# Performance work log

Measured on AMD Instinct MI355X. Metric: run time of the kernel, lower is better.

Reference implementation:

```python
import jax, jax.numpy as jnp
import numpy as np

EPS = 1e-5
PATCH_LEN, STRIDE, SEQ_LEN = 16, 8, 512
D_FF, N_HEADS = 32, 8


def setup_inputs() -> dict:
    key = jax.random.key(0)
    ks = jax.random.split(key, 16)
    d_model, d_llm, V, num_tok, pred_len = 32, 4096, 32000, 1000, 96
    hf = N_HEADS * D_FF  # 256
    patch_nums = (SEQ_LEN - PATCH_LEN) // STRIDE + 2  # 64
    head_nf = D_FF * patch_nums  # 2048
    r = lambda k, s, fan: jax.random.normal(k, s, jnp.float32) / np.sqrt(fan)
    return {
        'x_enc': jax.random.normal(ks[0], (32, SEQ_LEN, 7), jnp.float32),
        'conv_w': r(ks[1], (d_model, PATCH_LEN, 3), PATCH_LEN * 3),
        'word_emb': jax.random.normal(ks[2], (V, d_llm), jnp.float32) * 0.02,
        'map_w': r(ks[3], (num_tok, V), V),
        'map_b': jnp.zeros((num_tok,), jnp.float32),
        'wq': r(ks[4], (hf, d_model), d_model), 'bq': jnp.zeros((hf,), jnp.float32),
        'wk': r(ks[5], (hf, d_llm), d_llm), 'bk': jnp.zeros((hf,), jnp.float32),
        'wv': r(ks[6], (hf, d_llm), d_llm), 'bv': jnp.zeros((hf,), jnp.float32),
        'wo': r(ks[7], (d_llm, hf), hf), 'bo': jnp.zeros((d_llm,), jnp.float32),
        'head_w': r(ks[8], (pred_len, head_nf), head_nf),
        'head_b': jnp.zeros((pred_len,), jnp.float32),
    }


def _forward(x_enc, conv_w, word_emb, map_w, map_b, wq, bq, wk, bk, wv, bv, wo, bo, head_w, head_b):
    B, T, N = x_enc.shape
    # RevIN normalize (stats detached, as in torch)
    mean = jax.lax.stop_gradient(jnp.mean(x_enc, axis=1, keepdims=True))
    stdev = jax.lax.stop_gradient(jnp.sqrt(jnp.var(x_enc, axis=1, keepdims=True) + EPS))
    x = (x_enc - mean) / stdev                      # [B,T,N]

    # Patch embedding: [B,N,T] -> replication pad -> unfold -> circular conv
    xt = jnp.transpose(x, (0, 2, 1))                # [B,N,T]
    xt = jnp.concatenate([xt, jnp.repeat(xt[..., -1:], STRIDE, axis=-1)], axis=-1)  # [B,N,T+stride]
    starts = jnp.arange(0, T + STRIDE - PATCH_LEN + 1, STRIDE)
    idx = starts[:, None] + jnp.arange(PATCH_LEN)   # [L, patch_len]
    patches = xt[:, :, idx]                         # [B,N,L,patch_len]
    L = patches.shape[2]
    p = patches.reshape(B * N, L, PATCH_LEN)
    # TokenEmbedding: conv1d over patch axis, circular pad 1, no bias
    pc = jnp.transpose(p, (0, 2, 1))                # [BN, patch_len, L]
    pc = jnp.concatenate([pc[..., -1:], pc, pc[..., :1]], axis=-1)
    emb = jax.lax.conv_general_dilated(pc, conv_w, (1,), 'VALID',
                                       dimension_numbers=('NCH', 'OIH', 'NCH'))
    enc = jnp.transpose(emb, (0, 2, 1))             # [BN, L, d_model]

    # Source embeddings: mapping_layer(word_emb.T).T -> [num_tokens, d_llm]
    src = (word_emb.T @ map_w.T + map_b).T          # [num_tok, d_llm]

    # Reprogramming cross-attention
    BN = enc.shape[0]
    q = (enc @ wq.T + bq).reshape(BN, L, N_HEADS, D_FF)   # [BN,L,H,E]
    k = (src @ wk.T + bk).reshape(-1, N_HEADS, D_FF)      # [S,H,E]
    v = (src @ wv.T + bv).reshape(-1, N_HEADS, D_FF)      # [S,H,E]
    scale = 1.0 / np.sqrt(D_FF)
    scores = jnp.einsum('blhe,she->bhls', q, k)
    A = jax.nn.softmax(scale * scores, axis=-1)
    rep = jnp.einsum('bhls,she->blhe', A, v).reshape(BN, L, N_HEADS * D_FF)
    out = rep @ wo.T + bo                           # [BN, L, d_llm]

    # LLM stubbed as identity; keep first d_ff channels (Time-LLM post-LLM path)
    dec = out[..., :D_FF]                           # [BN, L, d_ff]
    dec = dec.reshape(B, N, L, D_FF).transpose(0, 1, 3, 2)  # [B,N,d_ff,L]
    dec = dec.reshape(B, N, D_FF * L)               # FlattenHead
    dec = dec @ head_w.T + head_b                   # [B,N,pred_len]
    dec = jnp.transpose(dec, (0, 2, 1))             # [B,pred_len,N]
    # RevIN denormalize
    return dec * stdev + mean


def reference(x_enc, conv_w, word_emb, map_w, map_b, wq, bq, wk, bk, wv, bv, wo, bo, head_w, head_b):
    return _forward(x_enc, conv_w, word_emb, map_w, map_b, wq, bq, wk, bk, wv, bv, wo, bo, head_w, head_b)
```

## Files before the change

### kernel.cpp

```cpp
#include <hip/hip_runtime.h>
#include <math.h>

constexpr int B_ = 32, T_ = 512, N_ = 7, BN_ = 224;
constexpr int L_ = 64, DM_ = 32, PLEN_ = 16;
constexpr int HF_ = 256, NH_ = 8, DFF_ = 32;
constexpr int S_ = 1000, SP_ = 1024, DLLM_ = 4096, V_ = 32000;
constexpr int PRED_ = 96, HNF_ = 2048;
constexpr int KSPLIT2 = 25, KCH2 = 1280;

typedef short bf16x8 __attribute__((ext_vector_type(8)));
typedef float f32x4 __attribute__((ext_vector_type(4)));

__device__ inline ushort f2bf(float x) {
    union { float f; uint u; } v; v.f = x;
    uint r = v.u + 0x7fffu + ((v.u >> 16) & 1u);
    return (ushort)(r >> 16);
}
__device__ inline uint pk(float a, float b) {
    return (uint)f2bf(a) | ((uint)f2bf(b) << 16);
}
__device__ inline void gl16(const void* g, void* l) {
    __builtin_amdgcn_global_load_lds(
        (const __attribute__((address_space(1))) void*)g,
        (__attribute__((address_space(3))) void*)l, 16, 0, 0);
}

__global__ __launch_bounds__(256) void k_pre(const float* __restrict__ x,
                                             const float* __restrict__ conv_w,
                                             const float* __restrict__ wq,
                                             const float* __restrict__ bq,
                                             float* __restrict__ mean_o,
                                             float* __restrict__ std_o,
                                             float* __restrict__ qo) {
    const int bn = blockIdx.x, b = bn / N_, n = bn % N_;
    __shared__ float xn[520];
    __shared__ float cw[DM_ * PLEN_ * 3];
    __shared__ float enc_s[2048];
    __shared__ float wqs[HF_ * DM_];
    __shared__ float rs[4], rq[4], sm2[2];
    const int tid = threadIdx.x;
    const float* xp = x + (size_t)b * T_ * N_ + n;

    float s = 0.f, sq = 0.f;
    for (int t = tid; t < T_; t += 256) { float v = xp[(size_t)t * N_]; s += v; sq += v * v; }
    for (int i = tid; i < DM_ * PLEN_ * 3; i += 256) cw[i] = conv_w[i];
    for (int i = tid; i < HF_ * DM_; i += 256) wqs[i] = wq[i];
    for (int o = 32; o > 0; o >>= 1) { s += __shfl_down(s, o, 64); sq += __shfl_down(sq, o, 64); }
    int wid = tid >> 6, lane = tid & 63;
    if (lane == 0) { rs[wid] = s; rq[wid] = sq; }
    __syncthreads();
    if (tid == 0) {
        float S = rs[0] + rs[1] + rs[2] + rs[3];
        float Q = rq[0] + rq[1] + rq[2] + rq[3];
        float m = S / T_;
        float var = Q / T_ - m * m;
        float sd = sqrtf(var + 1e-5f);
        mean_o[bn] = m; std_o[bn] = sd;
        sm2[0] = m; sm2[1] = sd;
    }
    __syncthreads();
    const float m = sm2[0], rstd = 1.0f / sm2[1];
    for (int t = tid; t < T_; t += 256) xn[t] = (xp[(size_t)t * N_] - m) * rstd;
    __syncthreads();
    if (tid < 8) xn[T_ + tid] = xn[T_ - 1];
    __syncthreads();
    for (int idx = tid; idx < L_ * DM_ * 8; idx += 256) { }
    for (int idx = tid; idx < L_ * DM_; idx += 256) {
        int l = idx >> 5, o = idx & 31;
        float acc = 0.f;
        #pragma unroll
        for (int t = 0; t < 3; t++) {
            int col = l + t;
            int pcol = (col == 0) ? 63 : ((col == 65) ? 0 : col - 1);
            const float* xb = &xn[pcol * 8];
            const float* cwb = &cw[o * 48 + t];
            #pragma unroll
            for (int i = 0; i < 16; i++) acc += xb[i] * cwb[i * 3];
        }
        enc_s[idx] = acc;
    }
    __syncthreads();
    const float scale = 0.17677669529663687f;
    for (int idx = tid; idx < L_ * HF_; idx += 256) {
        int l = idx >> 8, c = idx & 255;
        float acc = bq[c];
        const float* e = &enc_s[l * 32];
        const float* w = &wqs[c * 32];
        #pragma unroll
        for (int k = 0; k < 32; k++) acc += e[k] * w[k];
        qo[(size_t)bn * L_ * HF_ + idx] = acc * scale;
    }
}

__global__ __launch_bounds__(256) void k_wsum(const float* __restrict__ wk,
                                              const float* __restrict__ wv,
                                              float* __restrict__ wsum) {
    int c = blockIdx.x;
    const float* row = (c < HF_) ? wk + (size_t)c * DLLM_ : wv + (size_t)(c - HF_) * DLLM_;
    float s = 0.f;
    for (int d = threadIdx.x; d < DLLM_; d += 256) s += row[d];
    for (int o = 32; o > 0; o >>= 1) s += __shfl_down(s, o, 64);
    __shared__ float rs[4];
    int wid = threadIdx.x >> 6, lane = threadIdx.x & 63;
    if (lane == 0) rs[wid] = s;
    __syncthreads();
    if (threadIdx.x == 0) wsum[c] = rs[0] + rs[1] + rs[2] + rs[3];
}

__global__ __launch_bounds__(256) void k_cvt_wkv(const float* __restrict__ wk,
                                                 const float* __restrict__ wv,
                                                 ushort* __restrict__ out) {
    int g = blockIdx.x * 256 + threadIdx.x;
    int e = g * 8;
    const float* src = (e < HF_ * DLLM_) ? wk + e : wv + (e - HF_ * DLLM_);
    float4 x = *(const float4*)src, y = *(const float4*)(src + 4);
    uint4 w; w.x = pk(x.x, x.y); w.y = pk(x.z, x.w); w.z = pk(y.x, y.y); w.w = pk(y.z, y.w);
    *(uint4*)(out + e) = w;
}

__global__ __launch_bounds__(512) void k_gemm1(const float* __restrict__ A,
                                               const ushort* __restrict__ Bw,
                                               ushort* __restrict__ ET) {
    __shared__ union {
        struct { float Af[2][128 * 32]; ushort Bs[2][256 * 32]; } st;
        ushort C[256 * 72];
    } lds;
    const int tid = threadIdx.x;
    const int lane = tid & 63, wid = tid >> 6;
    const int wr = wid >> 2, wc = wid & 3;
    const int n0 = blockIdx.x * 256, m0 = blockIdx.y * 128;

    const int arw = tid >> 3, acq = (tid & 7) ^ ((tid >> 3) & 7);
    const float* asrc0 = A + (size_t)(m0 + arw) * DLLM_ + acq * 4;
    const float* asrc1 = asrc0 + (size_t)64 * DLLM_;

    const int u0 = tid, rb0 = u0 >> 2, ob0 = (u0 & 3) ^ ((rb0 >> 1) & 3);
    const int u1 = tid + 512, rb1 = u1 >> 2, ob1 = (u1 & 3) ^ ((rb1 >> 1) & 3);
    const ushort* bptr0 = Bw + (size_t)(n0 + rb0) * DLLM_ + ob0 * 8;
    const ushort* bptr1 = Bw + (size_t)(n0 + rb1) * DLLM_ + ob1 * 8;

    const int rl = lane & 15, g = lane >> 4;
    const int oc = g ^ ((rl >> 1) & 3);

    f32x4 acc[4][4];
    #pragma unroll
    for (int i = 0; i < 4; i++)
        #pragma unroll
        for (int j = 0; j < 4; j++) acc[i][j] = (f32x4){0.f, 0.f, 0.f, 0.f};

    gl16(asrc0, &lds.st.Af[0][tid * 4]);
    gl16(asrc1, &lds.st.Af[0][(tid + 512) * 4]);
    gl16(bptr0, &lds.st.Bs[0][u0 * 8]);
    gl16(bptr1, &lds.st.Bs[0][u1 * 8]);
    __syncthreads();

    int cur = 0;
    constexpr int NT = DLLM_ / 32;
    for (int t = 0; t < NT; ++t) {
        if (t + 1 < NT) {
            const int o = (t + 1) * 32;
            gl16(asrc0 + o, &lds.st.Af[cur ^ 1][tid * 4]);
            gl16(asrc1 + o, &lds.st.Af[cur ^ 1][(tid + 512) * 4]);
            gl16(bptr0 + o, &lds.st.Bs[cur ^ 1][u0 * 8]);
            gl16(bptr1 + o, &lds.st.Bs[cur ^ 1][u1 * 8]);
            asm volatile("s_waitcnt vmcnt(4)" ::: "memory");
        } else {
            asm volatile("s_waitcnt vmcnt(0)" ::: "memory");
        }
        __builtin_amdgcn_s_barrier();
        asm volatile("" ::: "memory");
        const float* Ab = lds.st.Af[cur];
        const ushort* Bb = lds.st.Bs[cur];
        bf16x8 af[4], bfr[4];
        #pragma unroll
        for (int mi = 0; mi < 4; mi++) {
            int row = wr * 64 + mi * 16 + rl;
            int s = row & 7;
            int ulo = row * 8 + ((2 * g) ^ s);
            int uhi = row * 8 + ((2 * g + 1) ^ s);
            f32x4 xlo = *(const f32x4*)&Ab[ulo * 4];
            f32x4 xhi = *(const f32x4*)&Ab[uhi * 4];
            uint4 w; w.x = pk(xlo[0], xlo[1]); w.y = pk(xlo[2], xlo[3]);
            w.z = pk(xhi[0], xhi[1]); w.w = pk(xhi[2], xhi[3]);
            union { uint4 u; bf16x8 b; } cv; cv.u = w;
            af[mi] = cv.b;
        }
        #pragma unroll
        for (int ni = 0; ni < 4; ni++)
            bfr[ni] = *(const bf16x8*)&Bb[(wc * 64 + ni * 16 + rl) * 32 + oc * 8];
        __builtin_amdgcn_s_setprio(1);
        #pragma unroll
        for (int mi = 0; mi < 4; mi++)
            #pragma unroll
            for (int ni = 0; ni < 4; ni++)
                acc[mi][ni] = __builtin_amdgcn_mfma_f32_16x16x32_bf16(af[mi], bfr[ni], acc[mi][ni], 0, 0, 0);
        __builtin_amdgcn_s_setprio(0);
        asm volatile("s_waitcnt lgkmcnt(0)" ::: "memory");
        __builtin_amdgcn_s_barrier();
        cur ^= 1;
    }

    #pragma unroll
    for (int p = 0; p < 2; p++) {
        __syncthreads();
        if (wr == p) {
            #pragma unroll
            for (int mi = 0; mi < 4; mi++)
                #pragma unroll
                for (int ni = 0; ni < 4; ni++) {
                    int nl = wc * 64 + ni * 16 + (lane & 15);
                    int ml = mi * 16 + (lane >> 4) * 4;
                    uint2 w2;
                    w2.x = pk(acc[mi][ni][0], acc[mi][ni][1]);
                    w2.y = pk(acc[mi][ni][2], acc[mi][ni][3]);
                    *(uint2*)&lds.C[nl * 72 + ml] = w2;
                }
        }
        __syncthreads();
        {
            int r = tid >> 1, half = tid & 1;
            const uint4* src = (const uint4*)&lds.C[r * 72 + half * 32];
            ushort* dst = ET + (size_t)(n0 + r) * V_ + m0 + p * 64 + half * 32;
            uint4 v0 = src[0], v1 = src[1], v2 = src[2], v3 = src[3];
            *(uint4*)(dst + 0) = v0; *(uint4*)(dst + 8) = v1;
            *(uint4*)(dst + 16) = v2; *(uint4*)(dst + 24) = v3;
        }
    }
}

__global__ __launch_bounds__(256) void k_gemm2(const float* __restrict__ A,
                                               const ushort* __restrict__ ET,
                                               float* __restrict__ Cp) {
    __shared__ float Af[2][128 * 32];
    __shared__ ushort Bs[2][128 * 32];
    const int tid = threadIdx.x, lane = tid & 63, wid = tid >> 6;
    const int wr = wid >> 1, wc = wid & 1;
    const int m0 = blockIdx.x * 128, n0 = blockIdx.y * 128, kz = blockIdx.z;
    const size_t kbase = (size_t)kz * KCH2;

    const float* asrc[4];
    #pragma unroll
    for (int i = 0; i < 4; i++) {
        int u = i * 256 + tid;
        int r = u >> 3, c = (u & 7) ^ (r & 7);
        int rm = m0 + r; if (rm > S_ - 1) rm = S_ - 1;
        asrc[i] = A + (size_t)rm * V_ + kbase + c * 4;
    }
    const int u0 = tid, rb0 = u0 >> 2, ob0 = (u0 & 3) ^ ((rb0 >> 1) & 3);
    const int u1 = tid + 256, rb1 = u1 >> 2, ob1 = (u1 & 3) ^ ((rb1 >> 1) & 3);
    const ushort* bp0 = ET + (size_t)(n0 + rb0) * V_ + kbase + ob0 * 8;
    const ushort* bp1 = ET + (size_t)(n0 + rb1) * V_ + kbase + ob1 * 8;

    const int rl = lane & 15, g = lane >> 4;
    const int oB = g ^ ((rl >> 1) & 3);

    f32x4 acc[4][4];
    #pragma unroll
    for (int i = 0; i < 4; i++)
        #pragma unroll
        for (int j = 0; j < 4; j++) acc[i][j] = (f32x4){0.f, 0.f, 0.f, 0.f};

    gl16(bp0, &Bs[0][u0 * 8]);
    gl16(bp1, &Bs[0][u1 * 8]);
    #pragma unroll
    for (int i = 0; i < 4; i++) gl16(asrc[i], &Af[0][(i * 256 + tid) * 4]);
    __syncthreads();

    int cur = 0;
    constexpr int NT = KCH2 / 32;
    for (int t = 0; t < NT; ++t) {
        if (t + 1 < NT) {
            const int o = (t + 1) * 32;
            gl16(bp0 + o, &Bs[cur ^ 1][u0 * 8]);
            gl16(bp1 + o, &Bs[cur ^ 1][u1 * 8]);
            #pragma unroll
            for (int i = 0; i < 4; i++) gl16(asrc[i] + o, &Af[cur ^ 1][(i * 256 + tid) * 4]);
            asm volatile("s_waitcnt vmcnt(6)" ::: "memory");
        } else {
            asm volatile("s_waitcnt vmcnt(0)" ::: "memory");
        }
        __builtin_amdgcn_s_barrier();
        asm volatile("" ::: "memory");
        const float* Ab = Af[cur];
        const ushort* Bb = Bs[cur];
        bf16x8 af[4], bfr[4];
        #pragma unroll
        for (int mi = 0; mi < 4; mi++) {
            int row = wr * 64 + mi * 16 + rl;
            int s = row & 7;
            int ulo = row * 8 + ((2 * g) ^ s);
            int uhi = row * 8 + ((2 * g + 1) ^ s);
            f32x4 xlo = *(const f32x4*)&Ab[ulo * 4];
            f32x4 xhi = *(const f32x4*)&Ab[uhi * 4];
            uint4 w; w.x = pk(xlo[0], xlo[1]); w.y = pk(xlo[2], xlo[3]);
            w.z = pk(xhi[0], xhi[1]); w.w = pk(xhi[2], xhi[3]);
            union { uint4 u; bf16x8 b; } cv; cv.u = w;
            af[mi] = cv.b;
        }
        #pragma unroll
        for (int ni = 0; ni < 4; ni++)
            bfr[ni] = *(const bf16x8*)&Bb[(wc * 64 + ni * 16 + rl) * 32 + oB * 8];
        __builtin_amdgcn_s_setprio(1);
        #pragma unroll
        for (int mi = 0; mi < 4; mi++)
            #pragma unroll
            for (int ni = 0; ni < 4; ni++)
                acc[mi][ni] = __builtin_amdgcn_mfma_f32_16x16x32_bf16(af[mi], bfr[ni], acc[mi][ni], 0, 0, 0);
        __builtin_amdgcn_s_setprio(0);
        asm volatile("s_waitcnt lgkmcnt(0)" ::: "memory");
        __builtin_amdgcn_s_barrier();
        cur ^= 1;
    }

    #pragma unroll
    for (int mi = 0; mi < 4; mi++)
        #pragma unroll
        for (int ni = 0; ni < 4; ni++)
            #pragma unroll
            for (int j = 0; j < 4; j++) {
                int m = m0 + wr * 64 + mi * 16 + (lane >> 4) * 4 + j;
                int n = n0 + wc * 64 + ni * 16 + (lane & 15);
                if (m < S_) Cp[((size_t)kz * S_ + m) * 512 + n] = acc[mi][ni][j];
            }
}

__global__ __launch_bounds__(256) void k_red(const float* __restrict__ Cp,
                                             const float* __restrict__ mb,
                                             const float* __restrict__ wsum,
                                             const float* __restrict__ bk,
                                             const float* __restrict__ bv,
                                             ushort* __restrict__ Kb,
                                             ushort* __restrict__ Vt) {
    int idx = blockIdx.x * 256 + threadIdx.x;
    if (idx >= SP_ * 512) return;
    int m = idx >> 9, n = idx & 511;
    float s = 0.f;
    if (m < S_) {
        #pragma unroll
        for (int z = 0; z < KSPLIT2; z++) s += Cp[(size_t)z * S_ * 512 + (size_t)m * 512 + n];
        float bias = (n < HF_) ? bk[n] : bv[n - HF_];
        s += mb[m] * wsum[n] + bias;
    }
    ushort h = f2bf(s);
    if (n < HF_) Kb[(size_t)m * HF_ + n] = h;
    else Vt[(size_t)(n - HF_) * SP_ + m] = h;
}

__global__ __launch_bounds__(256) void k_attn(const float* __restrict__ q,
                                              const ushort* __restrict__ Kb,
                                              const ushort* __restrict__ Vt,
                                              float* __restrict__ rep) {
    const int h = blockIdx.x, bn = blockIdx.y;
    __shared__ ushort Ks[2][64 * 32];
    __shared__ ushort Vs[2][32 * 64];
    __shared__ float  Ps[4][16 * 64];
    const int tid = threadIdx.x, lane = tid & 63, w = tid >> 6;
    const int rl = lane & 15, g = lane >> 4;

    const int krow = tid >> 2, koc = (tid & 3) ^ ((krow >> 1) & 3);
    const ushort* ksrc = Kb + (size_t)krow * HF_ + h * 32 + koc * 8;
    const int verow = tid >> 3, vso = (tid & 7) ^ (verow & 7);
    const ushort* vsrc = Vt + (size_t)(h * 32 + verow) * SP_ + vso * 8;

    bf16x8 qf;
    {
        const float* qp = q + ((size_t)bn * L_ + w * 16 + rl) * HF_ + h * 32 + g * 8;
        float4 x = *(const float4*)qp, y = *(const float4*)(qp + 4);
        uint4 u; u.x = pk(x.x, x.y); u.y = pk(x.z, x.w); u.z = pk(y.x, y.y); u.w = pk(y.z, y.w);
        union { uint4 u4; bf16x8 b; } cv; cv.u4 = u; qf = cv.b;
    }

    float mrow[4] = {-1e30f, -1e30f, -1e30f, -1e30f};
    float rsum[4] = {0.f, 0.f, 0.f, 0.f};
    f32x4 oacc[2] = {(f32x4){0,0,0,0}, (f32x4){0,0,0,0}};
    float* Pw = Ps[w];

    gl16(ksrc, &Ks[0][tid * 8]);
    gl16(vsrc, &Vs[0][tid * 8]);
    __syncthreads();

    int cur = 0;
    for (int t = 0; t < 16; ++t) {
        if (t + 1 < 16) {
            gl16(ksrc + (size_t)(t + 1) * 64 * HF_, &Ks[cur ^ 1][tid * 8]);
            gl16(vsrc + (t + 1) * 64, &Vs[cur ^ 1][tid * 8]);
            asm volatile("s_waitcnt vmcnt(2)" ::: "memory");
        } else {
            asm volatile("s_waitcnt vmcnt(0)" ::: "memory");
        }
        __builtin_amdgcn_s_barrier();
        asm volatile("" ::: "memory");
        const int s0 = t * 64;

        f32x4 sc[4];
        __builtin_amdgcn_s_setprio(1);
        #pragma unroll
        for (int nf = 0; nf < 4; nf++) {
            const int row = nf * 16 + rl;
            bf16x8 kf = *(const bf16x8*)&Ks[cur][(row * 4 + (g ^ ((rl >> 1) & 3))) * 8];
            sc[nf] = __builtin_amdgcn_mfma_f32_16x16x32_bf16(qf, kf, (f32x4){0, 0, 0, 0}, 0, 0, 0);
            if (s0 + row >= S_) sc[nf] = (f32x4){-1e30f, -1e30f, -1e30f, -1e30f};
        }
        __builtin_amdgcn_s_setprio(0);
        float tmax[4];
        #pragma unroll
        for (int j = 0; j < 4; j++)
            tmax[j] = fmaxf(fmaxf(sc[0][j], sc[1][j]), fmaxf(sc[2][j], sc[3][j]));
        #pragma unroll
        for (int d = 1; d < 16; d <<= 1)
            #pragma unroll
            for (int j = 0; j < 4; j++) tmax[j] = fmaxf(tmax[j], __shfl_xor(tmax[j], d, 64));
        float resc[4];
        #pragma unroll
        for (int j = 0; j < 4; j++) {
            float mn = fmaxf(mrow[j], tmax[j]);
            resc[j] = __expf(mrow[j] - mn);
            mrow[j] = mn;
            rsum[j] *= resc[j];
            oacc[0][j] *= resc[j];
            oacc[1][j] *= resc[j];
        }
        #pragma unroll
        for (int nf = 0; nf < 4; nf++) {
            const int s = nf * 16 + rl;
            #pragma unroll
            for (int j = 0; j < 4; j++) {
                float p = __expf(sc[nf][j] - mrow[j]);
                float pf = __uint_as_float(((uint)f2bf(p)) << 16);
                rsum[j] += pf;
                const int row = 4 * g + j;
                Pw[row * 64 + (((s >> 2) ^ row) << 2) + (s & 3)] = pf;
            }
        }
        __builtin_amdgcn_s_setprio(1);
        #pragma unroll
        for (int h2 = 0; h2 < 2; h2++) {
            const int q1 = (h2 * 8 + 2 * g) ^ rl;
            const int q2 = (h2 * 8 + 2 * g + 1) ^ rl;
            f32x4 plo = *(const f32x4*)&Pw[rl * 64 + q1 * 4];
            f32x4 phi = *(const f32x4*)&Pw[rl * 64 + q2 * 4];
            uint4 pu; pu.x = pk(plo[0], plo[1]); pu.y = pk(plo[2], plo[3]);
            pu.z = pk(phi[0], phi[1]); pu.w = pk(phi[2], phi[3]);
            union { uint4 u; bf16x8 b; } cv; cv.u = pu;
            bf16x8 pa = cv.b;
            #pragma unroll
            for (int eg = 0; eg < 2; eg++) {
                const int erow = eg * 16 + rl;
                const int su = (h2 * 4 + g) ^ (erow & 7);
                bf16x8 vf = *(const bf16x8*)&Vs[cur][erow * 64 + su * 8];
                oacc[eg] = __builtin_amdgcn_mfma_f32_16x16x32_bf16(pa, vf, oacc[eg], 0, 0, 0);
            }
        }
        __builtin_amdgcn_s_setprio(0);
        asm volatile("s_waitcnt lgkmcnt(0)" ::: "memory");
        __builtin_amdgcn_s_barrier();
        cur ^= 1;
    }

    #pragma unroll
    for (int d = 1; d < 16; d <<= 1)
        #pragma unroll
        for (int j = 0; j < 4; j++) rsum[j] += __shfl_xor(rsum[j], d, 64);
    float inv[4];
    #pragma unroll
    for (int j = 0; j < 4; j++) inv[j] = 1.0f / rsum[j];
    #pragma unroll
    for (int eg = 0; eg < 2; eg++)
        #pragma unroll
        for (int j = 0; j < 4; j++)
            rep[((size_t)bn * HF_ + h * 32 + eg * 16 + rl) * 64 + w * 16 + 4 * g + j] =
                oacc[eg][j] * inv[j];
}

__global__ __launch_bounds__(256) void k_post(const float* __restrict__ rep,
                                              const float* __restrict__ wo,
                                              const float* __restrict__ bo,
                                              const float* __restrict__ hw,
                                              const float* __restrict__ hb,
                                              const float* __restrict__ mean_i,
                                              const float* __restrict__ std_i,
                                              float* __restrict__ out) {
    const int bn = blockIdx.x, b = bn / N_, n = bn % N_;
    __shared__ float woT[HF_ * 32];
    __shared__ float dt[2048];
    const int tid = threadIdx.x;
    for (int idx = tid; idx < HF_ * 32; idx += 256) {
        int e = idx & 31, c = idx >> 5;
        woT[c * 32 + e] = wo[(size_t)e * HF_ + c];
    }
    __syncthreads();
    {
        const int l = tid & 63, e0 = (tid >> 6) * 8;
        float acc[8];
        #pragma unroll
        for (int i = 0; i < 8; i++) acc[i] = bo[e0 + i];
        const float* rp = rep + (size_t)bn * HF_ * 64 + l;
        for (int c = 0; c < HF_; c++) {
            float rv = rp[(size_t)c * 64];
            #pragma unroll
            for (int i = 0; i < 8; i++) acc[i] += rv * woT[c * 32 + e0 + i];
        }
        #pragma unroll
        for (int i = 0; i < 8; i++) dt[l * 32 + e0 + i] = acc[i];
    }
    __syncthreads();
    const float m = mean_i[bn], sd = std_i[bn];
    for (int p = tid; p < PRED_; p += 256) {
        float acc = hb[p];
        const float* w = hw + (size_t)p * HNF_;
        for (int f = 0; f < DFF_; f++) {
            const float* wf = w + f * 64;
            #pragma unroll
            for (int ll = 0; ll < 64; ll++) acc += dt[ll * 32 + f] * wf[ll];
        }
        out[(size_t)b * PRED_ * N_ + (size_t)p * N_ + n] = acc * sd + m;
    }
}

extern "C" void kernel_launch(void* const* d_in, const int* in_sizes, int n_in,
                              void* d_out, int out_size, void* d_ws, size_t ws_size,
                              hipStream_t stream) {
    const float* x_enc   = (const float*)d_in[0];
    const float* conv_w  = (const float*)d_in[1];
    const float* word_emb= (const float*)d_in[2];
    const float* map_w   = (const float*)d_in[3];
    const float* map_b   = (const float*)d_in[4];
    const float* wq      = (const float*)d_in[5];
    const float* bq      = (const float*)d_in[6];
    const float* wk      = (const float*)d_in[7];
    const float* bk      = (const float*)d_in[8];
    const float* wv      = (const float*)d_in[9];
    const float* bv      = (const float*)d_in[10];
    const float* wo      = (const float*)d_in[11];
    const float* bo      = (const float*)d_in[12];
    const float* head_w  = (const float*)d_in[13];
    const float* head_b  = (const float*)d_in[14];

    float* ws = (float*)d_ws;
    float* mean_w = ws;
    float* std_w  = ws + 256;
    float* wsum_w = ws + 512;
    float* q_w    = ws + 1024;
    float* kv_w   = q_w + (size_t)BN_ * L_ * HF_;
    float* cp_w   = kv_w + (size_t)S_ * 512;
    float* rep_w  = cp_w;
    ushort* et_w  = (ushort*)(cp_w + (size_t)KSPLIT2 * S_ * 512);
    ushort* wkv_w = et_w + (size_t)512 * V_;
    ushort* kb_w  = (ushort*)kv_w;
    ushort* vt_w  = kb_w + (size_t)SP_ * HF_;

    k_pre<<<BN_, 256, 0, stream>>>(x_enc, conv_w, wq, bq, mean_w, std_w, q_w);
    k_wsum<<<512, 256, 0, stream>>>(wk, wv, wsum_w);
    k_cvt_wkv<<<(512 * DLLM_ / 8) / 256, 256, 0, stream>>>(wk, wv, wkv_w);
    k_gemm1<<<dim3(2, V_ / 128), 512, 0, stream>>>(word_emb, wkv_w, et_w);
    k_gemm2<<<dim3(8, 4, KSPLIT2), 256, 0, stream>>>(map_w, et_w, cp_w);
    k_red<<<(SP_ * 512) / 256, 256, 0, stream>>>(cp_w, map_b, wsum_w, bk, bv, kb_w, vt_w);
    k_attn<<<dim3(NH_, BN_), 256, 0, stream>>>(q_w, kb_w, vt_w, rep_w);
    k_post<<<BN_, 256, 0, stream>>>(rep_w, wo, bo, head_w, head_b, mean_w, std_w, (float*)d_out);
}
```

Measured before the change: 555.2 us.

## Convert GEMM A tile to bf16 on store and single-buffer attention K/V

In the K/V projection GEMM, the fp32 A tile is now loaded into registers, converted to bf16, and written to LDS after the MFMAs, instead of being copied to LDS as fp32 and converted on every fragment read. This halves the LDS footprint and traffic for A and removes repeated conversions, but the global load now goes through registers and the loop waits for all loads with one barrier per step. The attention kernel drops K/V double buffering and loads each tile synchronously before computing, which frees LDS and may raise occupancy at the cost of exposed load latency. An empty dead loop in the prep kernel is also removed.

```diff
diff --git a/kernel.cpp b/kernel.cpp
--- a/kernel.cpp
+++ b/kernel.cpp
@@ -64,7 +64,6 @@
     __syncthreads();
     if (tid < 8) xn[T_ + tid] = xn[T_ - 1];
     __syncthreads();
-    for (int idx = tid; idx < L_ * DM_ * 8; idx += 256) { }
     for (int idx = tid; idx < L_ * DM_; idx += 256) {
         int l = idx >> 5, o = idx & 31;
         float acc = 0.f;
@@ -122,7 +121,7 @@
                                                const ushort* __restrict__ Bw,
                                                ushort* __restrict__ ET) {
     __shared__ union {
-        struct { float Af[2][128 * 32]; ushort Bs[2][256 * 32]; } st;
+        struct { ushort A2[2][128 * 32]; ushort Bs[2][256 * 32]; } st;
         ushort C[256 * 72];
     } lds;
     const int tid = threadIdx.x;
@@ -130,9 +129,9 @@
     const int wr = wid >> 2, wc = wid & 3;
     const int n0 = blockIdx.x * 256, m0 = blockIdx.y * 128;
 
-    const int arw = tid >> 3, acq = (tid & 7) ^ ((tid >> 3) & 7);
-    const float* asrc0 = A + (size_t)(m0 + arw) * DLLM_ + acq * 4;
-    const float* asrc1 = asrc0 + (size_t)64 * DLLM_;
+    const int ar = tid >> 2, ao = tid & 3;
+    const int au = (ar << 2) | (ao ^ ((ar >> 1) & 3));
+    const float* aptr = A + (size_t)(m0 + ar) * DLLM_ + ao * 8;
 
     const int u0 = tid, rb0 = u0 >> 2, ob0 = (u0 & 3) ^ ((rb0 >> 1) & 3);
     const int u1 = tid + 512, rb1 = u1 >> 2, ob1 = (u1 & 3) ^ ((rb1 >> 1) & 3);
@@ -148,42 +147,36 @@
         #pragma unroll
         for (int j = 0; j < 4; j++) acc[i][j] = (f32x4){0.f, 0.f, 0.f, 0.f};
 
-    gl16(asrc0, &lds.st.Af[0][tid * 4]);
-    gl16(asrc1, &lds.st.Af[0][(tid + 512) * 4]);
+    float4 pa0 = *(const float4*)aptr;
+    float4 pa1 = *(const float4*)(aptr + 4);
     gl16(bptr0, &lds.st.Bs[0][u0 * 8]);
     gl16(bptr1, &lds.st.Bs[0][u1 * 8]);
+    {
+        uint4 wa; wa.x = pk(pa0.x, pa0.y); wa.y = pk(pa0.z, pa0.w);
+        wa.z = pk(pa1.x, pa1.y); wa.w = pk(pa1.z, pa1.w);
+        *(uint4*)&lds.st.A2[0][au * 8] = wa;
+    }
     __syncthreads();
 
     int cur = 0;
     constexpr int NT = DLLM_ / 32;
     for (int t = 0; t < NT; ++t) {
-        if (t + 1 < NT) {
+        const bool more = (t + 1 < NT);
+        if (more) {
             const int o = (t + 1) * 32;
-            gl16(asrc0 + o, &lds.st.Af[cur ^ 1][tid * 4]);
-            gl16(asrc1 + o, &lds.st.Af[cur ^ 1][(tid + 512) * 4]);
+            const float* ap = aptr + o;
+            pa0 = *(const float4*)ap;
+            pa1 = *(const float4*)(ap + 4);
             gl16(bptr0 + o, &lds.st.Bs[cur ^ 1][u0 * 8]);
             gl16(bptr1 + o, &lds.st.Bs[cur ^ 1][u1 * 8]);
-            asm volatile("s_waitcnt vmcnt(4)" ::: "memory");
-        } else {
-            asm volatile("s_waitcnt vmcnt(0)" ::: "memory");
-        }
-        __builtin_amdgcn_s_barrier();
-        asm volatile("" ::: "memory");
-        const float* Ab = lds.st.Af[cur];
+        }
+        const ushort* Ab = lds.st.A2[cur];
         const ushort* Bb = lds.st.Bs[cur];
         bf16x8 af[4], bfr[4];
         #pragma unroll
         for (int mi = 0; mi < 4; mi++) {
             int row = wr * 64 + mi * 16 + rl;
-            int s = row & 7;
-            int ulo = row * 8 + ((2 * g) ^ s);
-            int uhi = row * 8 + ((2 * g + 1) ^ s);
-            f32x4 xlo = *(const f32x4*)&Ab[ulo * 4];
-            f32x4 xhi = *(const f32x4*)&Ab[uhi * 4];
-            uint4 w; w.x = pk(xlo[0], xlo[1]); w.y = pk(xlo[2], xlo[3]);
-            w.z = pk(xhi[0], xhi[1]); w.w = pk(xhi[2], xhi[3]);
-            union { uint4 u; bf16x8 b; } cv; cv.u = w;
-            af[mi] = cv.b;
+            af[mi] = *(const bf16x8*)&Ab[(row * 4 + oc) * 8];
         }
         #pragma unroll
         for (int ni = 0; ni < 4; ni++)
@@ -195,8 +188,14 @@
             for (int ni = 0; ni < 4; ni++)
                 acc[mi][ni] = __builtin_amdgcn_mfma_f32_16x16x32_bf16(af[mi], bfr[ni], acc[mi][ni], 0, 0, 0);
         __builtin_amdgcn_s_setprio(0);
-        asm volatile("s_waitcnt lgkmcnt(0)" ::: "memory");
+        if (more) {
+            uint4 wa; wa.x = pk(pa0.x, pa0.y); wa.y = pk(pa0.z, pa0.w);
+            wa.z = pk(pa1.x, pa1.y); wa.w = pk(pa1.z, pa1.w);
+            *(uint4*)&lds.st.A2[cur ^ 1][au * 8] = wa;
+        }
+        asm volatile("s_waitcnt vmcnt(0) lgkmcnt(0)" ::: "memory");
         __builtin_amdgcn_s_barrier();
+        asm volatile("" ::: "memory");
         cur ^= 1;
     }
 
@@ -351,16 +350,18 @@
                                               const ushort* __restrict__ Vt,
                                               float* __restrict__ rep) {
     const int h = blockIdx.x, bn = blockIdx.y;
-    __shared__ ushort Ks[2][64 * 32];
-    __shared__ ushort Vs[2][32 * 64];
+    __shared__ ushort Ks[64 * 32];
+    __shared__ ushort Vs[32 * 64];
     __shared__ float  Ps[4][16 * 64];
     const int tid = threadIdx.x, lane = tid & 63, w = tid >> 6;
     const int rl = lane & 15, g = lane >> 4;
 
     const int krow = tid >> 2, koc = (tid & 3) ^ ((krow >> 1) & 3);
     const ushort* ksrc = Kb + (size_t)krow * HF_ + h * 32 + koc * 8;
+    ushort* kdst = &Ks[tid * 8];
     const int verow = tid >> 3, vso = (tid & 7) ^ (verow & 7);
     const ushort* vsrc = Vt + (size_t)(h * 32 + verow) * SP_ + vso * 8;
+    ushort* vdst = &Vs[tid * 8];
 
     bf16x8 qf;
     {
@@ -375,29 +376,18 @@
     f32x4 oacc[2] = {(f32x4){0,0,0,0}, (f32x4){0,0,0,0}};
     float* Pw = Ps[w];
 
-    gl16(ksrc, &Ks[0][tid * 8]);
-    gl16(vsrc, &Vs[0][tid * 8]);
-    __syncthreads();
-
-    int cur = 0;
     for (int t = 0; t < 16; ++t) {
-        if (t + 1 < 16) {
-            gl16(ksrc + (size_t)(t + 1) * 64 * HF_, &Ks[cur ^ 1][tid * 8]);
-            gl16(vsrc + (t + 1) * 64, &Vs[cur ^ 1][tid * 8]);
-            asm volatile("s_waitcnt vmcnt(2)" ::: "memory");
-        } else {
-            asm volatile("s_waitcnt vmcnt(0)" ::: "memory");
-        }
-        __builtin_amdgcn_s_barrier();
-        asm volatile("" ::: "memory");
         const int s0 = t * 64;
+        gl16(ksrc + (size_t)s0 * HF_, kdst);
+        gl16(vsrc + s0, vdst);
+        __syncthreads();
 
         f32x4 sc[4];
         __builtin_amdgcn_s_setprio(1);
         #pragma unroll
         for (int nf = 0; nf < 4; nf++) {
             const int row = nf * 16 + rl;
-            bf16x8 kf = *(const bf16x8*)&Ks[cur][(row * 4 + (g ^ ((rl >> 1) & 3))) * 8];
+            bf16x8 kf = *(const bf16x8*)&Ks[(row * 4 + (g ^ ((rl >> 1) & 3))) * 8];
             sc[nf] = __builtin_amdgcn_mfma_f32_16x16x32_bf16(qf, kf, (f32x4){0, 0, 0, 0}, 0, 0, 0);
             if (s0 + row >= S_) sc[nf] = (f32x4){-1e30f, -1e30f, -1e30f, -1e30f};
         }
@@ -447,14 +437,12 @@
             for (int eg = 0; eg < 2; eg++) {
                 const int erow = eg * 16 + rl;
                 const int su = (h2 * 4 + g) ^ (erow & 7);
-                bf16x8 vf = *(const bf16x8*)&Vs[cur][erow * 64 + su * 8];
+                bf16x8 vf = *(const bf16x8*)&Vs[erow * 64 + su * 8];
                 oacc[eg] = __builtin_amdgcn_mfma_f32_16x16x32_bf16(pa, vf, oacc[eg], 0, 0, 0);
             }
         }
         __builtin_amdgcn_s_setprio(0);
-        asm volatile("s_waitcnt lgkmcnt(0)" ::: "memory");
-        __builtin_amdgcn_s_barrier();
-        cur ^= 1;
+        __syncthreads();
     }
 
     #pragma unroll
```

Result: faster. 536.6 us (-3.4%).
